# Kernel optimization log

Measured on AMD Instinct MI355X. Metric: run time of the kernel, lower is better.

Reference implementation:

```python
import jax, jax.numpy as jnp
import numpy as np

B, S, H = 32, 2048, 1024


def setup_inputs() -> dict:
    key = jax.random.key(0)
    ks = jax.random.split(key, 7)
    return {
        "query": jax.random.normal(ks[0], (B, 1, H), dtype=jnp.float32),
        "key": jax.random.normal(ks[1], (S, B, H), dtype=jnp.float32),
        "Wa_w": jax.random.normal(ks[2], (H, H), dtype=jnp.float32) / np.sqrt(H),
        "Wa_b": jax.random.normal(ks[3], (H,), dtype=jnp.float32) * 0.01,
        "Ua_w": jax.random.normal(ks[4], (H, H), dtype=jnp.float32) / np.sqrt(H),
        "Ua_b": jax.random.normal(ks[5], (H,), dtype=jnp.float32) * 0.01,
        "va_w": jax.random.normal(ks[6], (H,), dtype=jnp.float32) / np.sqrt(H),
        "va_b": jnp.zeros((1,), dtype=jnp.float32),
    }


def reference(query, key, Wa_w, Wa_b, Ua_w, Ua_b, va_w, va_b):
    # key: (S, B, H) -> (B, S, H)
    k = jnp.transpose(key, (1, 0, 2))
    # additive (Bahdanau) energies: tanh(Wa q + Ua k), broadcast over S
    e = jnp.tanh((query @ Wa_w + Wa_b) + (k @ Ua_w + Ua_b))  # (B, S, H)
    scores = jnp.einsum("bsh,h->bs", e, va_w) + va_b[0]       # (B, S)
    weights = jax.nn.softmax(scores, axis=-1)[:, None, :]      # (B, 1, S)
    context = jnp.einsum("bqs,bsh->bqh", weights, k)           # (B, 1, H)
    return context, weights
```

## Files before the change

### kernel.cpp

```cpp
#include <hip/hip_runtime.h>

#define Hdim 1024
#define Bdim 32
#define Sdim 2048

typedef __attribute__((ext_vector_type(8))) __bf16 bf16x8;
typedef __attribute__((ext_vector_type(4))) float f32x4;

#define GLOAD_LDS16(gp, lp)                                                              \
  __builtin_amdgcn_global_load_lds(                                                     \
      (const __attribute__((address_space(1))) unsigned int*)(gp),                      \
      (__attribute__((address_space(3))) unsigned int*)(lp), 16, 0, 0)

__global__ __launch_bounds__(256) void convert_key_kernel(const float* __restrict__ key,
                                                          __bf16* __restrict__ bkey) {
  size_t idx = (size_t)blockIdx.x * 256 + threadIdx.x;
  const float4* src = (const float4*)(key + idx * 8);
  float4 f0 = src[0], f1 = src[1];
  bf16x8 t;
  t[0] = (__bf16)f0.x; t[1] = (__bf16)f0.y; t[2] = (__bf16)f0.z; t[3] = (__bf16)f0.w;
  t[4] = (__bf16)f1.x; t[5] = (__bf16)f1.y; t[6] = (__bf16)f1.z; t[7] = (__bf16)f1.w;
  *(bf16x8*)(bkey + idx * 8) = t;
}

__global__ __launch_bounds__(256) void convert_ua_kernel(const float* __restrict__ Ua,
                                                         __bf16* __restrict__ ubt) {
  int du = blockIdx.x * 256 + threadIdx.x;
  int n  = du & 127;
  int k8 = (du >> 7) & 127;
  int nt = du >> 14;
  int ng = nt * 128 + n;
  bf16x8 t;
#pragma unroll
  for (int j = 0; j < 8; ++j)
    t[j] = (__bf16)Ua[(k8 * 8 + j) * Hdim + ng];
  *(bf16x8*)(ubt + (size_t)du * 8) = t;
}

__global__ __launch_bounds__(256) void qc_kernel(const float* __restrict__ q,
                                                 const float* __restrict__ Wa,
                                                 const float* __restrict__ Wab,
                                                 const float* __restrict__ Uab,
                                                 float* __restrict__ qc) {
  int b = blockIdx.y;
  int h = blockIdx.x * 256 + threadIdx.x;
  float acc = Wab[h] + Uab[h];
  const float* qr = q + b * Hdim;
#pragma unroll 16
  for (int i = 0; i < Hdim; ++i)
    acc = fmaf(qr[i], Wa[i * Hdim + h], acc);
  qc[b * Hdim + h] = acc;
}

__global__ __launch_bounds__(256) void gemm_scores_bf16_kernel(const __bf16* __restrict__ bkey,
                                                               const __bf16* __restrict__ ubt,
                                                               const float* __restrict__ qc,
                                                               const float* __restrict__ va,
                                                               float* __restrict__ part) {
  __shared__ __align__(16) __bf16 ABs[8192];
  __shared__ float red[256];

  const int tid  = threadIdx.x;
  const int w    = tid >> 6;
  const int lane = tid & 63;
  const int quad = lane >> 4;
  const int l16  = lane & 15;

  const int l   = blockIdx.x;
  const int xcd = l & 7;
  const int i2  = l >> 3;
  const int mt  = xcd * 64 + (i2 >> 3);
  const int nt  = i2 & 7;

  const int r0 = mt * 128;
  const int n0 = nt * 128;
  const int wm = (w & 1) * 64;
  const int wn = (w >> 1) * 64;

  __bf16* As = ABs;
  __bf16* Bs = ABs + 4096;

  f32x4 acc[4][4] = {};

  for (int kc = 0; kc < Hdim; kc += 32) {
#pragma unroll
    for (int it = 0; it < 2; ++it) {
      int u  = it * 256 + tid;
      int k8 = u >> 7, row = u & 127;
      GLOAD_LDS16(bkey + (size_t)(r0 + row) * Hdim + kc + k8 * 8, As + u * 8);
    }
#pragma unroll
    for (int it = 0; it < 2; ++it) {
      int u = it * 256 + tid;
      GLOAD_LDS16(ubt + ((size_t)nt * 16384 + (kc >> 3) * 128 + u) * 8, Bs + u * 8);
    }
    __syncthreads();

    bf16x8 afr[4], bfr[4];
#pragma unroll
    for (int i = 0; i < 4; ++i)
      afr[i] = *(const bf16x8*)&As[(quad * 128 + wm + i * 16 + l16) * 8];
#pragma unroll
    for (int j = 0; j < 4; ++j)
      bfr[j] = *(const bf16x8*)&Bs[(quad * 128 + wn + j * 16 + l16) * 8];

#pragma unroll
    for (int i = 0; i < 4; ++i)
#pragma unroll
      for (int j = 0; j < 4; ++j)
        acc[i][j] = __builtin_amdgcn_mfma_f32_16x16x32_bf16(afr[i], bfr[j], acc[i][j], 0, 0, 0);

    __syncthreads();
  }

  float* qcs = (float*)ABs;
#pragma unroll
  for (int it = 0; it < 16; ++it) {
    int u = it * 256 + tid;
    qcs[u] = qc[(u >> 7) * Hdim + n0 + (u & 127)];
  }
  __syncthreads();

  float vav[4];
#pragma unroll
  for (int j = 0; j < 4; ++j) vav[j] = va[n0 + wn + j * 16 + l16];

#pragma unroll
  for (int i = 0; i < 4; ++i) {
#pragma unroll
    for (int rg = 0; rg < 4; ++rg) {
      int b = (i & 1) * 16 + quad * 4 + rg;
      float sum = 0.f;
#pragma unroll
      for (int j = 0; j < 4; ++j) {
        float v = acc[i][j][rg] + qcs[b * 128 + wn + j * 16 + l16];
        v = fminf(fmaxf(v, -15.f), 15.f);
        float e = __expf(2.f * v);
        sum += (e - 1.f) * __builtin_amdgcn_rcpf(e + 1.f) * vav[j];
      }
#pragma unroll
      for (int off = 1; off < 16; off <<= 1)
        sum += __shfl_xor(sum, off, 64);
      if (l16 == 0)
        red[(wm + i * 16 + quad * 4 + rg) * 2 + (w >> 1)] = sum;
    }
  }
  __syncthreads();
  if (tid < 128)
    part[(size_t)(r0 + tid) * 8 + nt] = red[tid * 2] + red[tid * 2 + 1];
}

__global__ __launch_bounds__(256) void gemm_scores_kernel(const float* __restrict__ key,
                                                          const __bf16* __restrict__ ubt,
                                                          const float* __restrict__ qc,
                                                          const float* __restrict__ va,
                                                          float* __restrict__ part) {
  __shared__ __align__(16) float AsQ[4096];
  __shared__ __align__(16) __bf16 Bs[4096];
  __shared__ float red[256];

  const int tid  = threadIdx.x;
  const int w    = tid >> 6;
  const int lane = tid & 63;
  const int quad = lane >> 4;
  const int l16  = lane & 15;
  const int l   = blockIdx.x;
  const int xcd = l & 7;
  const int i2  = l >> 3;
  const int mt  = xcd * 64 + (i2 >> 3);
  const int nt  = i2 & 7;
  const int r0 = mt * 128;
  const int n0 = nt * 128;
  const int wm = (w & 1) * 64;
  const int wn = (w >> 1) * 64;

  f32x4 acc[4][4] = {};

  for (int kc = 0; kc < Hdim; kc += 32) {
#pragma unroll
    for (int it = 0; it < 4; ++it) {
      int u  = it * 256 + tid;
      int k4 = u >> 7, row = u & 127;
      GLOAD_LDS16(key + (size_t)(r0 + row) * Hdim + kc + k4 * 4, AsQ + u * 4);
    }
#pragma unroll
    for (int it = 0; it < 2; ++it) {
      int u = it * 256 + tid;
      GLOAD_LDS16(ubt + ((size_t)nt * 16384 + (kc >> 3) * 128 + u) * 8, Bs + u * 8);
    }
    __syncthreads();

    bf16x8 bfr[4];
#pragma unroll
    for (int j = 0; j < 4; ++j)
      bfr[j] = *(const bf16x8*)&Bs[(quad * 128 + wn + j * 16 + l16) * 8];

    bf16x8 afr[4];
#pragma unroll
    for (int i = 0; i < 4; ++i) {
      int ml = wm + i * 16 + l16;
      float4 f0 = *(const float4*)&AsQ[((quad * 2) * 128 + ml) * 4];
      float4 f1 = *(const float4*)&AsQ[((quad * 2 + 1) * 128 + ml) * 4];
      bf16x8 a;
      a[0] = (__bf16)f0.x; a[1] = (__bf16)f0.y; a[2] = (__bf16)f0.z; a[3] = (__bf16)f0.w;
      a[4] = (__bf16)f1.x; a[5] = (__bf16)f1.y; a[6] = (__bf16)f1.z; a[7] = (__bf16)f1.w;
      afr[i] = a;
    }

#pragma unroll
    for (int i = 0; i < 4; ++i)
#pragma unroll
      for (int j = 0; j < 4; ++j)
        acc[i][j] = __builtin_amdgcn_mfma_f32_16x16x32_bf16(afr[i], bfr[j], acc[i][j], 0, 0, 0);

    __syncthreads();
  }

#pragma unroll
  for (int it = 0; it < 16; ++it) {
    int u = it * 256 + tid;
    AsQ[u] = qc[(u >> 7) * Hdim + n0 + (u & 127)];
  }
  __syncthreads();

  float vav[4];
#pragma unroll
  for (int j = 0; j < 4; ++j) vav[j] = va[n0 + wn + j * 16 + l16];

#pragma unroll
  for (int i = 0; i < 4; ++i) {
#pragma unroll
    for (int rg = 0; rg < 4; ++rg) {
      int b = (i & 1) * 16 + quad * 4 + rg;
      float sum = 0.f;
#pragma unroll
      for (int j = 0; j < 4; ++j) {
        float v = acc[i][j][rg] + AsQ[b * 128 + wn + j * 16 + l16];
        v = fminf(fmaxf(v, -15.f), 15.f);
        float e = __expf(2.f * v);
        sum += (e - 1.f) * __builtin_amdgcn_rcpf(e + 1.f) * vav[j];
      }
#pragma unroll
      for (int off = 1; off < 16; off <<= 1)
        sum += __shfl_xor(sum, off, 64);
      if (l16 == 0)
        red[(wm + i * 16 + quad * 4 + rg) * 2 + (w >> 1)] = sum;
    }
  }
  __syncthreads();
  if (tid < 128)
    part[(size_t)(r0 + tid) * 8 + nt] = red[tid * 2] + red[tid * 2 + 1];
}

__global__ __launch_bounds__(256) void softmax_kernel(const float* __restrict__ part,
                                                      float* __restrict__ dout) {
  int b = blockIdx.x, t = threadIdx.x;
  int w = t >> 6, lane = t & 63;
  __shared__ float red1[4], red2[4];
  float sc[8];
  float m = -1e30f;
#pragma unroll
  for (int c = 0; c < 8; ++c) {
    int s = c * 256 + t;
    const float4* p = (const float4*)&part[(size_t)(s * 32 + b) * 8];
    float4 p0 = p[0], p1 = p[1];
    float v = ((p0.x + p0.y) + (p0.z + p0.w)) + ((p1.x + p1.y) + (p1.z + p1.w));
    sc[c] = v;
    m = fmaxf(m, v);
  }
#pragma unroll
  for (int off = 1; off < 64; off <<= 1) m = fmaxf(m, __shfl_xor(m, off, 64));
  if (lane == 0) red1[w] = m;
  __syncthreads();
  m = fmaxf(fmaxf(red1[0], red1[1]), fmaxf(red1[2], red1[3]));
  float sum = 0.f;
#pragma unroll
  for (int c = 0; c < 8; ++c) { sc[c] = __expf(sc[c] - m); sum += sc[c]; }
#pragma unroll
  for (int off = 1; off < 64; off <<= 1) sum += __shfl_xor(sum, off, 64);
  if (lane == 0) red2[w] = sum;
  __syncthreads();
  float inv = 1.f / (red2[0] + red2[1] + red2[2] + red2[3]);
#pragma unroll
  for (int c = 0; c < 8; ++c)
    dout[32768 + b * 2048 + c * 256 + t] = sc[c] * inv;
}

__global__ __launch_bounds__(256) void ctx_part_kernel(const float* __restrict__ key,
                                                       const float* __restrict__ dout,
                                                       float* __restrict__ cpart) {
  int sc = blockIdx.x;
  int b  = blockIdx.y;
  int t  = threadIdx.x;
  float4 acc = make_float4(0.f, 0.f, 0.f, 0.f);
  int s0 = sc * 64;
#pragma unroll 8
  for (int s = s0; s < s0 + 64; ++s) {
    float wgt = dout[32768 + b * 2048 + s];
    float4 k4 = *(const float4*)&key[((size_t)(s * 32 + b) << 10) + t * 4];
    acc.x = fmaf(wgt, k4.x, acc.x);
    acc.y = fmaf(wgt, k4.y, acc.y);
    acc.z = fmaf(wgt, k4.z, acc.z);
    acc.w = fmaf(wgt, k4.w, acc.w);
  }
  *(float4*)&cpart[((size_t)(sc * 32 + b) << 10) + t * 4] = acc;
}

__global__ __launch_bounds__(256) void ctx_reduce_kernel(const float* __restrict__ cpart,
                                                         float* __restrict__ dout) {
  int o = blockIdx.x * 256 + threadIdx.x;
  int b = o >> 10, h = o & 1023;
  float s = 0.f;
#pragma unroll
  for (int sc = 0; sc < 32; ++sc)
    s += cpart[((size_t)(sc * 32 + b) << 10) + h];
  dout[o] = s;
}

extern "C" void kernel_launch(void* const* d_in, const int* in_sizes, int n_in,
                              void* d_out, int out_size, void* d_ws, size_t ws_size,
                              hipStream_t stream) {
  const float* q   = (const float*)d_in[0];
  const float* key = (const float*)d_in[1];
  const float* Waw = (const float*)d_in[2];
  const float* Wab = (const float*)d_in[3];
  const float* Uaw = (const float*)d_in[4];
  const float* Uab = (const float*)d_in[5];
  const float* vaw = (const float*)d_in[6];
  float* out = (float*)d_out;

  char* ws = (char*)d_ws;
  float*  qc    = (float*)(ws);
  __bf16* ubt   = (__bf16*)(ws + 131072);
  float*  part  = (float*)(ws + 131072 + 2097152);
  float*  cpart = (float*)(ws + 131072 + 2097152 + 2097152);
  __bf16* bkey  = (__bf16*)(ws + 131072 + 2097152 + 2097152 + 4194304);
  const size_t need = 131072ull + 2097152 + 2097152 + 4194304 + 134217728;

  convert_ua_kernel<<<512, 256, 0, stream>>>(Uaw, ubt);
  qc_kernel<<<dim3(4, 32), 256, 0, stream>>>(q, Waw, Wab, Uab, qc);
  if (ws_size >= need) {
    convert_key_kernel<<<32768, 256, 0, stream>>>(key, bkey);
    gemm_scores_bf16_kernel<<<4096, 256, 0, stream>>>(bkey, ubt, qc, vaw, part);
  } else {
    gemm_scores_kernel<<<4096, 256, 0, stream>>>(key, ubt, qc, vaw, part);
  }
  softmax_kernel<<<32, 256, 0, stream>>>(part, out);
  ctx_part_kernel<<<dim3(32, 32), 256, 0, stream>>>(key, out, cpart);
  ctx_reduce_kernel<<<128, 256, 0, stream>>>(cpart, out);
}
```

Measured before the change: 715.9 us.

## Double-buffer LDS tiles in bf16 score GEMM and transpose partial-score layout

The bf16 score GEMM now uses two LDS buffers, issuing global-to-LDS loads for the next K chunk before the MFMAs on the current chunk, so load latency can hide behind compute and one barrier per iteration is dropped. Separately, both GEMM kernels write partial scores in a batch-major [b][s] layout, and softmax reads that layout so each block streams contiguous memory. The cost is double the LDS per block, which may lower occupancy.

```diff
diff --git a/kernel.cpp b/kernel.cpp
--- a/kernel.cpp
+++ b/kernel.cpp
@@ -57,7 +57,7 @@
                                                                const float* __restrict__ qc,
                                                                const float* __restrict__ va,
                                                                float* __restrict__ part) {
-  __shared__ __align__(16) __bf16 ABs[8192];
+  __shared__ __align__(16) __bf16 AB[2][8192];
   __shared__ float red[256];
 
   const int tid  = threadIdx.x;
@@ -77,25 +77,44 @@
   const int wm = (w & 1) * 64;
   const int wn = (w >> 1) * 64;
 
-  __bf16* As = ABs;
-  __bf16* Bs = ABs + 4096;
+  const int uA0 = tid;
+  const int uA1 = 256 + tid;
+  const size_t baseB = (size_t)nt * 16384;
 
   f32x4 acc[4][4] = {};
 
+#pragma unroll
+  for (int it = 0; it < 2; ++it) {
+    int u = it * 256 + tid;
+    int k8 = u >> 7, row = u & 127;
+    GLOAD_LDS16(bkey + (size_t)(r0 + row) * Hdim + k8 * 8, AB[0] + u * 8);
+  }
+#pragma unroll
+  for (int it = 0; it < 2; ++it) {
+    int u = it * 256 + tid;
+    GLOAD_LDS16(ubt + (baseB + u) * 8, AB[0] + 4096 + u * 8);
+  }
+  __syncthreads();
+
+  int cur = 0;
   for (int kc = 0; kc < Hdim; kc += 32) {
-#pragma unroll
-    for (int it = 0; it < 2; ++it) {
-      int u  = it * 256 + tid;
-      int k8 = u >> 7, row = u & 127;
-      GLOAD_LDS16(bkey + (size_t)(r0 + row) * Hdim + kc + k8 * 8, As + u * 8);
-    }
-#pragma unroll
-    for (int it = 0; it < 2; ++it) {
-      int u = it * 256 + tid;
-      GLOAD_LDS16(ubt + ((size_t)nt * 16384 + (kc >> 3) * 128 + u) * 8, Bs + u * 8);
-    }
-    __syncthreads();
-
+    if (kc + 32 < Hdim) {
+      const int kn = kc + 32;
+#pragma unroll
+      for (int it = 0; it < 2; ++it) {
+        int u = it * 256 + tid;
+        int k8 = u >> 7, row = u & 127;
+        GLOAD_LDS16(bkey + (size_t)(r0 + row) * Hdim + kn + k8 * 8, AB[cur ^ 1] + u * 8);
+      }
+#pragma unroll
+      for (int it = 0; it < 2; ++it) {
+        int u = it * 256 + tid;
+        GLOAD_LDS16(ubt + (baseB + (kn >> 3) * 128 + u) * 8, AB[cur ^ 1] + 4096 + u * 8);
+      }
+    }
+
+    const __bf16* As = AB[cur];
+    const __bf16* Bs = AB[cur] + 4096;
     bf16x8 afr[4], bfr[4];
 #pragma unroll
     for (int i = 0; i < 4; ++i)
@@ -111,9 +130,10 @@
         acc[i][j] = __builtin_amdgcn_mfma_f32_16x16x32_bf16(afr[i], bfr[j], acc[i][j], 0, 0, 0);
 
     __syncthreads();
-  }
-
-  float* qcs = (float*)ABs;
+    cur ^= 1;
+  }
+
+  float* qcs = (float*)AB[0];
 #pragma unroll
   for (int it = 0; it < 16; ++it) {
     int u = it * 256 + tid;
@@ -146,8 +166,11 @@
     }
   }
   __syncthreads();
-  if (tid < 128)
-    part[(size_t)(r0 + tid) * 8 + nt] = red[tid * 2] + red[tid * 2 + 1];
+  if (tid < 128) {
+    int row = r0 + tid;
+    int bb = row & 31, ss = row >> 5;
+    part[((size_t)bb * Sdim + ss) * 8 + nt] = red[tid * 2] + red[tid * 2 + 1];
+  }
 }
 
 __global__ __launch_bounds__(256) void gemm_scores_kernel(const float* __restrict__ key,
@@ -248,8 +271,11 @@
     }
   }
   __syncthreads();
-  if (tid < 128)
-    part[(size_t)(r0 + tid) * 8 + nt] = red[tid * 2] + red[tid * 2 + 1];
+  if (tid < 128) {
+    int row = r0 + tid;
+    int bb = row & 31, ss = row >> 5;
+    part[((size_t)bb * Sdim + ss) * 8 + nt] = red[tid * 2] + red[tid * 2 + 1];
+  }
 }
 
 __global__ __launch_bounds__(256) void softmax_kernel(const float* __restrict__ part,
@@ -262,7 +288,7 @@
 #pragma unroll
   for (int c = 0; c < 8; ++c) {
     int s = c * 256 + t;
-    const float4* p = (const float4*)&part[(size_t)(s * 32 + b) * 8];
+    const float4* p = (const float4*)&part[((size_t)b * Sdim + s) * 8];
     float4 p0 = p[0], p1 = p[1];
     float v = ((p0.x + p0.y) + (p0.z + p0.w)) + ((p1.x + p1.y) + (p1.z + p1.w));
     sc[c] = v;
```

Result: no change. 706.1 us (-1.4%).

## Load MFMA operands directly from global into registers with double buffering

Applied to the files above, without the earlier changes.

The bf16 scores GEMM no longer stages A and B tiles through LDS with global_load_lds and per-iteration barriers. Each lane now loads its MFMA fragments straight from global memory into registers, using a two-stage register double buffer so the loads for the next k-slice are issued while the current MFMAs run. The partial-score buffer is also changed to a batch-major layout so the softmax kernel reads it contiguously. Operand reuse across warps through LDS is lost, which raises global and L2 traffic, and register pressure goes up.

```diff
diff --git a/kernel.cpp b/kernel.cpp
--- a/kernel.cpp
+++ b/kernel.cpp
@@ -57,7 +57,7 @@
                                                                const float* __restrict__ qc,
                                                                const float* __restrict__ va,
                                                                float* __restrict__ part) {
-  __shared__ __align__(16) __bf16 ABs[8192];
+  __shared__ float qcs[4096];
   __shared__ float red[256];
 
   const int tid  = threadIdx.x;
@@ -77,43 +77,50 @@
   const int wm = (w & 1) * 64;
   const int wn = (w >> 1) * 64;
 
-  __bf16* As = ABs;
-  __bf16* Bs = ABs + 4096;
+  const __bf16* Abase = bkey + ((size_t)(r0 + wm + l16)) * Hdim + quad * 8;
+  const __bf16* Bbase = ubt + ((size_t)nt * 16384 + (size_t)quad * 128 + wn + l16) * 8;
 
   f32x4 acc[4][4] = {};
-
-  for (int kc = 0; kc < Hdim; kc += 32) {
-#pragma unroll
-    for (int it = 0; it < 2; ++it) {
-      int u  = it * 256 + tid;
-      int k8 = u >> 7, row = u & 127;
-      GLOAD_LDS16(bkey + (size_t)(r0 + row) * Hdim + kc + k8 * 8, As + u * 8);
-    }
-#pragma unroll
-    for (int it = 0; it < 2; ++it) {
-      int u = it * 256 + tid;
-      GLOAD_LDS16(ubt + ((size_t)nt * 16384 + (kc >> 3) * 128 + u) * 8, Bs + u * 8);
-    }
-    __syncthreads();
-
-    bf16x8 afr[4], bfr[4];
+  bf16x8 aA[4], bA[4], aB[4], bB[4];
+
+#pragma unroll
+  for (int i = 0; i < 4; ++i) aA[i] = *(const bf16x8*)(Abase + (size_t)i * 16 * Hdim);
+#pragma unroll
+  for (int j = 0; j < 4; ++j) bA[j] = *(const bf16x8*)(Bbase + (size_t)j * 128);
+
+#pragma unroll
+  for (int s = 0; s < 16; ++s) {
+    const int k0 = s * 64;
 #pragma unroll
     for (int i = 0; i < 4; ++i)
-      afr[i] = *(const bf16x8*)&As[(quad * 128 + wm + i * 16 + l16) * 8];
+      aB[i] = *(const bf16x8*)(Abase + (size_t)i * 16 * Hdim + k0 + 32);
 #pragma unroll
     for (int j = 0; j < 4; ++j)
-      bfr[j] = *(const bf16x8*)&Bs[(quad * 128 + wn + j * 16 + l16) * 8];
+      bB[j] = *(const bf16x8*)(Bbase + (size_t)(k0 + 32) * 128 + (size_t)j * 128);
 
 #pragma unroll
     for (int i = 0; i < 4; ++i)
 #pragma unroll
       for (int j = 0; j < 4; ++j)
-        acc[i][j] = __builtin_amdgcn_mfma_f32_16x16x32_bf16(afr[i], bfr[j], acc[i][j], 0, 0, 0);
-
-    __syncthreads();
-  }
-
-  float* qcs = (float*)ABs;
+        acc[i][j] = __builtin_amdgcn_mfma_f32_16x16x32_bf16(aA[i], bA[j], acc[i][j], 0, 0, 0);
+
+    if (s < 15) {
+      const int k1 = k0 + 64;
+#pragma unroll
+      for (int i = 0; i < 4; ++i)
+        aA[i] = *(const bf16x8*)(Abase + (size_t)i * 16 * Hdim + k1);
+#pragma unroll
+      for (int j = 0; j < 4; ++j)
+        bA[j] = *(const bf16x8*)(Bbase + (size_t)k1 * 128 + (size_t)j * 128);
+    }
+
+#pragma unroll
+    for (int i = 0; i < 4; ++i)
+#pragma unroll
+      for (int j = 0; j < 4; ++j)
+        acc[i][j] = __builtin_amdgcn_mfma_f32_16x16x32_bf16(aB[i], bB[j], acc[i][j], 0, 0, 0);
+  }
+
 #pragma unroll
   for (int it = 0; it < 16; ++it) {
     int u = it * 256 + tid;
@@ -146,8 +153,11 @@
     }
   }
   __syncthreads();
-  if (tid < 128)
-    part[(size_t)(r0 + tid) * 8 + nt] = red[tid * 2] + red[tid * 2 + 1];
+  if (tid < 128) {
+    int row = r0 + tid;
+    int bb = row & 31, ss = row >> 5;
+    part[((size_t)bb * Sdim + ss) * 8 + nt] = red[tid * 2] + red[tid * 2 + 1];
+  }
 }
 
 __global__ __launch_bounds__(256) void gemm_scores_kernel(const float* __restrict__ key,
@@ -248,8 +258,11 @@
     }
   }
   __syncthreads();
-  if (tid < 128)
-    part[(size_t)(r0 + tid) * 8 + nt] = red[tid * 2] + red[tid * 2 + 1];
+  if (tid < 128) {
+    int row = r0 + tid;
+    int bb = row & 31, ss = row >> 5;
+    part[((size_t)bb * Sdim + ss) * 8 + nt] = red[tid * 2] + red[tid * 2 + 1];
+  }
 }
 
 __global__ __launch_bounds__(256) void softmax_kernel(const float* __restrict__ part,
@@ -262,7 +275,7 @@
 #pragma unroll
   for (int c = 0; c < 8; ++c) {
     int s = c * 256 + t;
-    const float4* p = (const float4*)&part[(size_t)(s * 32 + b) * 8];
+    const float4* p = (const float4*)&part[((size_t)b * Sdim + s) * 8];
     float4 p0 = p[0], p1 = p[1];
     float v = ((p0.x + p0.y) + (p0.z + p0.w)) + ((p1.x + p1.y) + (p1.z + p1.w));
     sc[c] = v;
```

Result: slower. 859.0 us (+20.0%).
